# Performance work log

Hardware: AMD Instinct MI355X
Metric: run time of the kernel (lower is better)

Reference implementation:

```python
import jax, jax.numpy as jnp
import numpy as np

HIDDEN = 1024
NUM_EXPERTS = 8
TOP_K = 2
BATCH, SEQ = 4, 2048


def setup_inputs() -> dict:
    key = jax.random.key(0)
    ks = jax.random.split(key, 7)
    s = 0.02
    x = jax.random.normal(ks[0], (BATCH, SEQ, HIDDEN), dtype=jnp.float32)
    Wr = jax.random.normal(ks[1], (HIDDEN, NUM_EXPERTS), dtype=jnp.float32) * s
    br = jnp.zeros((NUM_EXPERTS,), dtype=jnp.float32)
    W1 = jax.random.normal(ks[2], (NUM_EXPERTS, HIDDEN, 2 * HIDDEN), dtype=jnp.float32) * s
    b1 = jnp.zeros((NUM_EXPERTS, 2 * HIDDEN), dtype=jnp.float32)
    W2 = jax.random.normal(ks[3], (NUM_EXPERTS, 2 * HIDDEN, HIDDEN), dtype=jnp.float32) * s
    b2 = jnp.zeros((NUM_EXPERTS, HIDDEN), dtype=jnp.float32)
    return {"x": x, "Wr": Wr, "br": br, "W1": W1, "b1": b1, "W2": W2, "b2": b2}


def reference(x, Wr, br, W1, b1, W2, b2):
    # Router: softmax over experts, take top-k, renormalize top-k weights.
    logits = jnp.einsum('bsh,he->bse', x, Wr) + br              # [B,S,E]
    routing = jax.nn.softmax(logits, axis=-1)
    topw, topi = jax.lax.top_k(routing, TOP_K)                   # [B,S,K]
    topw = jax.nn.softmax(topw, axis=-1)
    # Dense all-expert MLP (same math as masked gather/scatter combine).
    h = jnp.einsum('bsh,ehf->bsef', x, W1) + b1                  # [B,S,E,2H]
    h = jax.nn.gelu(h, approximate=False)                        # torch GELU = exact erf
    y = jnp.einsum('bsef,efh->bseh', h, W2) + b2                 # [B,S,E,H]
    # Per-token expert combine weights: sum_k onehot(topi_k)*topw_k -> [B,S,E]
    scale = jnp.sum(jax.nn.one_hot(topi, NUM_EXPERTS, dtype=x.dtype) * topw[..., None], axis=-2)
    return jnp.einsum('bse,bseh->bsh', scale, y)
```

## Files before the change

kernel.cpp:

```cpp
#include <hip/hip_runtime.h>
#include <math.h>

#define HID 1024
#define FF  2048
#define NE  8
#define NT  8192

typedef __attribute__((ext_vector_type(4))) float f32x4;
typedef __bf16 bf16x8 __attribute__((ext_vector_type(8)));

#define GLL(g, l) __builtin_amdgcn_global_load_lds( \
    (const __attribute__((address_space(1))) unsigned int*)(g), \
    (__attribute__((address_space(3))) unsigned int*)(l), 16, 0, 0)

static __device__ __forceinline__ ushort f2b(float f){
  union { float f; unsigned int u; } v; v.f = f;
  unsigned int r = (v.u + 0x7FFFu + ((v.u >> 16) & 1u)) >> 16;
  return (ushort)r;
}

__global__ __launch_bounds__(256) void k_cvt_x(const float* __restrict__ x,
                                               ushort* __restrict__ xb){
  size_t i8 = ((size_t)blockIdx.x * 256 + threadIdx.x) * 8;
  const float* s = x + i8;
  ushort o[8];
  #pragma unroll
  for (int j = 0; j < 8; ++j) o[j] = f2b(s[j]);
  *(uint4*)(xb + i8) = *(uint4*)o;
}

__global__ __launch_bounds__(256) void k_transpose(
    const float* __restrict__ src, ushort* __restrict__ dst, int K, int N){
  __shared__ __align__(16) ushort Tt[64][72];
  int e = blockIdx.z;
  int n0 = blockIdx.x * 64, k0 = blockIdx.y * 64;
  int t = threadIdx.x;
  int r = t >> 2, c = (t & 3) * 16;
  const float* s = src + (size_t)e*K*N + (size_t)(k0+r)*N + n0 + c;
  #pragma unroll
  for (int q = 0; q < 4; ++q){
    float4 v = *(const float4*)(s + q*4);
    Tt[r][c+q*4+0] = f2b(v.x); Tt[r][c+q*4+1] = f2b(v.y);
    Tt[r][c+q*4+2] = f2b(v.z); Tt[r][c+q*4+3] = f2b(v.w);
  }
  __syncthreads();
  ushort tmp[16];
  #pragma unroll
  for (int i = 0; i < 16; ++i) tmp[i] = Tt[c+i][r];
  ushort* d = dst + (size_t)e*N*K + (size_t)(n0+r)*K + k0 + c;
  *(uint4*)(d)     = *(uint4*)&tmp[0];
  *(uint4*)(d + 8) = *(uint4*)&tmp[8];
}

__global__ __launch_bounds__(256) void k_router(
    const float* __restrict__ x, const float* __restrict__ Wr,
    const float* __restrict__ br, int* __restrict__ topi,
    float* __restrict__ topw){
  __shared__ __align__(16) float sW[HID*NE];
  int tid = threadIdx.x;
  const uint4* srcW = (const uint4*)Wr;
  uint4* dstW = (uint4*)sW;
  #pragma unroll
  for (int i = 0; i < 8; ++i) dstW[tid*8+i] = srcW[tid*8+i];
  __syncthreads();
  int wave = tid >> 6, lane = tid & 63;
  int t = blockIdx.x * 4 + wave;
  const float* xrow = x + (size_t)t * HID;
  double acc[NE];
  #pragma unroll
  for (int e=0;e<NE;++e) acc[e]=0.0;
  for (int it = 0; it < HID/64; ++it){
    int h = it*64 + lane;
    double xv = (double)xrow[h];
    #pragma unroll
    for (int e=0;e<NE;++e) acc[e] += xv * (double)sW[h*NE+e];
  }
  #pragma unroll
  for (int off=32; off>0; off>>=1){
    #pragma unroll
    for (int e=0;e<NE;++e) acc[e] += __shfl_down(acc[e], off, 64);
  }
  if (lane == 0){
    double lg[NE], p[NE];
    double m = -1e300;
    #pragma unroll
    for (int e=0;e<NE;++e){ lg[e] = acc[e] + (double)br[e]; m = fmax(m, lg[e]); }
    double s = 0.0;
    #pragma unroll
    for (int e=0;e<NE;++e){ p[e] = exp(lg[e]-m); s += p[e]; }
    double inv = 1.0 / s;
    #pragma unroll
    for (int e=0;e<NE;++e) p[e] *= inv;
    int i0 = 0;
    #pragma unroll
    for (int e=1;e<NE;++e) if (p[e] > p[i0]) i0 = e;
    int i1 = -1;
    #pragma unroll
    for (int e=0;e<NE;++e){ if (e==i0) continue; if (i1 < 0 || p[e] > p[i1]) i1 = e; }
    double d = exp(p[i1] - p[i0]);
    topi[t*2+0] = i0; topi[t*2+1] = i1;
    topw[t*2+0] = (float)(1.0 / (1.0 + d));
    topw[t*2+1] = (float)(d / (1.0 + d));
  }
}

__global__ __launch_bounds__(256) void k_count(
    const int* __restrict__ topi, int* __restrict__ counts){
  __shared__ int lcnt[NE];
  int tid = threadIdx.x;
  if (tid < NE) lcnt[tid] = 0;
  __syncthreads();
  int t = blockIdx.x * 256 + tid;
  atomicAdd(&lcnt[topi[t*2+0]], 1);
  atomicAdd(&lcnt[topi[t*2+1]], 1);
  __syncthreads();
  if (tid < NE) atomicAdd(&counts[tid], lcnt[tid]);
}

__global__ void k_offsets(const int* __restrict__ counts, int* __restrict__ offsets,
                          int* __restrict__ cursor){
  if (threadIdx.x == 0 && blockIdx.x == 0){
    int run = 0;
    for (int e=0;e<NE;++e){ offsets[e] = run; cursor[e] = run; run += counts[e]; }
  }
}

__global__ __launch_bounds__(256) void k_fill(
    const int* __restrict__ topi, const float* __restrict__ topw, int* __restrict__ cursor,
    int* __restrict__ tok_of, float* __restrict__ w_of){
  __shared__ int lcnt[NE];
  __shared__ int lbase[NE];
  int tid = threadIdx.x;
  if (tid < NE) lcnt[tid] = 0;
  __syncthreads();
  int t = blockIdx.x * 256 + tid;
  int e0 = topi[t*2+0], e1 = topi[t*2+1];
  int p0 = atomicAdd(&lcnt[e0], 1);
  int p1 = atomicAdd(&lcnt[e1], 1);
  __syncthreads();
  if (tid < NE) lbase[tid] = atomicAdd(&cursor[tid], lcnt[tid]);
  __syncthreads();
  int pos0 = lbase[e0] + p0;
  tok_of[pos0] = t; w_of[pos0] = topw[t*2+0];
  int pos1 = lbase[e1] + p1;
  tok_of[pos1] = t; w_of[pos1] = topw[t*2+1];
}

__global__ __launch_bounds__(256) void k_gemm1(
    const ushort* __restrict__ x, const ushort* __restrict__ w1t, const float* __restrict__ b1,
    const int* __restrict__ tok_of, const int* __restrict__ offsets, const int* __restrict__ counts,
    ushort* __restrict__ hbuf){
  int e = blockIdx.z;
  int cnt = counts[e];
  int m0 = blockIdx.y * 128;
  if (m0 >= cnt) return;
  int n0 = blockIdx.x * 128;
  int base = offsets[e];
  __shared__ __align__(16) ushort As[128][32];
  __shared__ __align__(16) ushort Bs[128][32];
  int tid = threadIdx.x;
  int wave = tid >> 6, lane = tid & 63;
  int srow0 = wave*32 + (lane >> 2);
  int srow1 = srow0 + 16;
  int chunk = (lane & 3) * 8;
  int t0 = tok_of[base + min(m0 + srow0, cnt-1)];
  int t1 = tok_of[base + min(m0 + srow1, cnt-1)];
  const ushort* agp0 = x + (size_t)t0*HID + chunk;
  const ushort* agp1 = x + (size_t)t1*HID + chunk;
  const ushort* wb = w1t + (size_t)e*FF*HID;
  const ushort* bgp0 = wb + (size_t)(n0 + srow0)*HID + chunk;
  const ushort* bgp1 = wb + (size_t)(n0 + srow1)*HID + chunk;
  ushort* alds0 = &As[wave*32][0];
  ushort* alds1 = &As[wave*32+16][0];
  ushort* blds0 = &Bs[wave*32][0];
  ushort* blds1 = &Bs[wave*32+16][0];
  f32x4 acc[4][4];
  #pragma unroll
  for (int i=0;i<4;++i)
    #pragma unroll
    for (int j=0;j<4;++j){ acc[i][j][0]=0.f; acc[i][j][1]=0.f; acc[i][j][2]=0.f; acc[i][j][3]=0.f; }
  int wr = (wave >> 1) * 64, wc = (wave & 1) * 64;
  int lrow = lane & 15, quad = lane >> 4;
  for (int kk = 0; kk < HID; kk += 32){
    GLL(agp0 + kk, alds0);
    GLL(agp1 + kk, alds1);
    GLL(bgp0 + kk, blds0);
    GLL(bgp1 + kk, blds1);
    __syncthreads();
    bf16x8 af[4], bfr[4];
    #pragma unroll
    for (int i=0;i<4;++i) af[i]  = *(const bf16x8*)&As[wr + i*16 + lrow][quad*8];
    #pragma unroll
    for (int j=0;j<4;++j) bfr[j] = *(const bf16x8*)&Bs[wc + j*16 + lrow][quad*8];
    #pragma unroll
    for (int i=0;i<4;++i)
      #pragma unroll
      for (int j=0;j<4;++j)
        acc[i][j] = __builtin_amdgcn_mfma_f32_16x16x32_bf16(af[i], bfr[j], acc[i][j], 0, 0, 0);
    __syncthreads();
  }
  #pragma unroll
  for (int i=0;i<4;++i){
    #pragma unroll
    for (int rr=0; rr<4; ++rr){
      int mrel = wr + i*16 + quad*4 + rr;
      if (m0 + mrel < cnt){
        size_t grow = (size_t)(base + m0 + mrel) * FF;
        #pragma unroll
        for (int j=0;j<4;++j){
          int n = n0 + wc + j*16 + lrow;
          float v = acc[i][j][rr] + b1[e*FF + n];
          float g = 0.5f * v * (1.0f + erff(v * 0.70710678118654752f));
          hbuf[grow + n] = f2b(g);
        }
      }
    }
  }
}

__global__ __launch_bounds__(256) void k_gemm2(
    const ushort* __restrict__ hbuf, const ushort* __restrict__ w2t, const float* __restrict__ b2,
    const int* __restrict__ tok_of, const float* __restrict__ w_of,
    const int* __restrict__ offsets, const int* __restrict__ counts,
    float* __restrict__ outp){
  int e = blockIdx.z;
  int cnt = counts[e];
  int m0 = blockIdx.y * 128;
  if (m0 >= cnt) return;
  int n0 = blockIdx.x * 128;
  int base = offsets[e];
  __shared__ __align__(16) ushort As[128][32];
  __shared__ __align__(16) ushort Bs[128][32];
  int tid = threadIdx.x;
  int wave = tid >> 6, lane = tid & 63;
  int srow0 = wave*32 + (lane >> 2);
  int srow1 = srow0 + 16;
  int chunk = (lane & 3) * 8;
  int ar0 = base + min(m0 + srow0, cnt-1);
  int ar1 = base + min(m0 + srow1, cnt-1);
  const ushort* agp0 = hbuf + (size_t)ar0*FF + chunk;
  const ushort* agp1 = hbuf + (size_t)ar1*FF + chunk;
  const ushort* wb = w2t + (size_t)e*HID*FF;
  const ushort* bgp0 = wb + (size_t)(n0 + srow0)*FF + chunk;
  const ushort* bgp1 = wb + (size_t)(n0 + srow1)*FF + chunk;
  ushort* alds0 = &As[wave*32][0];
  ushort* alds1 = &As[wave*32+16][0];
  ushort* blds0 = &Bs[wave*32][0];
  ushort* blds1 = &Bs[wave*32+16][0];
  f32x4 acc[4][4];
  #pragma unroll
  for (int i=0;i<4;++i)
    #pragma unroll
    for (int j=0;j<4;++j){ acc[i][j][0]=0.f; acc[i][j][1]=0.f; acc[i][j][2]=0.f; acc[i][j][3]=0.f; }
  int wr = (wave >> 1) * 64, wc = (wave & 1) * 64;
  int lrow = lane & 15, quad = lane >> 4;
  for (int kk = 0; kk < FF; kk += 32){
    GLL(agp0 + kk, alds0);
    GLL(agp1 + kk, alds1);
    GLL(bgp0 + kk, blds0);
    GLL(bgp1 + kk, blds1);
    __syncthreads();
    bf16x8 af[4], bfr[4];
    #pragma unroll
    for (int i=0;i<4;++i) af[i]  = *(const bf16x8*)&As[wr + i*16 + lrow][quad*8];
    #pragma unroll
    for (int j=0;j<4;++j) bfr[j] = *(const bf16x8*)&Bs[wc + j*16 + lrow][quad*8];
    #pragma unroll
    for (int i=0;i<4;++i)
      #pragma unroll
      for (int j=0;j<4;++j)
        acc[i][j] = __builtin_amdgcn_mfma_f32_16x16x32_bf16(af[i], bfr[j], acc[i][j], 0, 0, 0);
    __syncthreads();
  }
  #pragma unroll
  for (int i=0;i<4;++i){
    #pragma unroll
    for (int rr=0; rr<4; ++rr){
      int mrel = wr + i*16 + quad*4 + rr;
      if (m0 + mrel < cnt){
        int pos = base + m0 + mrel;
        int tok = tok_of[pos];
        float wgt = w_of[pos];
        float* orow = outp + (size_t)tok * HID;
        #pragma unroll
        for (int j=0;j<4;++j){
          int n = n0 + wc + j*16 + lrow;
          float y = acc[i][j][rr] + b2[e*HID + n];
          atomicAdd(&orow[n], wgt * y);
        }
      }
    }
  }
}

extern "C" void kernel_launch(void* const* d_in, const int* in_sizes, int n_in,
                              void* d_out, int out_size, void* d_ws, size_t ws_size,
                              hipStream_t stream) {
  const float* x  = (const float*)d_in[0];
  const float* Wr = (const float*)d_in[1];
  const float* br = (const float*)d_in[2];
  const float* W1 = (const float*)d_in[3];
  const float* b1 = (const float*)d_in[4];
  const float* W2 = (const float*)d_in[5];
  const float* b2 = (const float*)d_in[6];
  float* out = (float*)d_out;

  char* w = (char*)d_ws;
  int*   counts  = (int*)(w + 0);
  int*   cursor  = (int*)(w + 64);
  int*   offsets = (int*)(w + 128);
  int*   topi    = (int*)(w + 131072);
  float* topw    = (float*)(w + 196608);
  int*   tok_of  = (int*)(w + 262144);
  float* w_of    = (float*)(w + 327680);
  const size_t XB_OFF  = 524288ull;
  const size_t W1T_OFF = XB_OFF  + 16ull*1024*1024;
  const size_t W2T_OFF = W1T_OFF + 32ull*1024*1024;
  const size_t HB_OFF  = W2T_OFF + 32ull*1024*1024;
  ushort* xb   = (ushort*)(w + XB_OFF);
  ushort* W1t  = (ushort*)(w + W1T_OFF);
  ushort* W2t  = (ushort*)(w + W2T_OFF);
  ushort* hbuf = (ushort*)(w + HB_OFF);

  hipMemsetAsync(w, 0, 256, stream);
  hipMemsetAsync(out, 0, (size_t)NT*HID*sizeof(float), stream);

  k_cvt_x<<<4096, 256, 0, stream>>>(x, xb);
  k_transpose<<<dim3(FF/64, HID/64, NE), 256, 0, stream>>>(W1, W1t, HID, FF);
  k_transpose<<<dim3(HID/64, FF/64, NE), 256, 0, stream>>>(W2, W2t, FF, HID);

  k_router<<<NT/4, 256, 0, stream>>>(x, Wr, br, topi, topw);
  k_count<<<NT/256, 256, 0, stream>>>(topi, counts);
  k_offsets<<<1, 64, 0, stream>>>(counts, offsets, cursor);
  k_fill<<<NT/256, 256, 0, stream>>>(topi, topw, cursor, tok_of, w_of);

  k_gemm1<<<dim3(FF/128, NT/128, NE), 256, 0, stream>>>(xb, W1t, b1, tok_of, offsets, counts, hbuf);
  k_gemm2<<<dim3(HID/128, NT/128, NE), 256, 0, stream>>>(hbuf, W2t, b2, tok_of, w_of, offsets, counts, out);
}
```

Before: 552.4 us.

## Compact expert tile scheduling and double-buffer LDS loads in MoE GEMMs

Builds a compact list of (expert, row-tile) pairs in the offsets kernel so both grouped GEMMs launch only about 136 live row tiles instead of a 64x8 grid where most blocks exit early. It also double-buffers the LDS tiles: the next K-slice is loaded asynchronously while the current one feeds MFMA, and one of the two barriers per iteration is removed. This is meant to cut launch and idle-block overhead and to hide global-load latency, at the cost of doubled LDS use per block. The single-barrier scheme relies on the barrier at the top of each iteration to order buffer reuse.

```diff
diff --git a/kernel.cpp b/kernel.cpp
--- a/kernel.cpp
+++ b/kernel.cpp
@@ -5,6 +5,7 @@
 #define FF  2048
 #define NE  8
 #define NT  8192
+#define MAXTILE 160
 
 typedef __attribute__((ext_vector_type(4))) float f32x4;
 typedef __bf16 bf16x8 __attribute__((ext_vector_type(8)));
@@ -118,10 +119,16 @@
 }
 
 __global__ void k_offsets(const int* __restrict__ counts, int* __restrict__ offsets,
-                          int* __restrict__ cursor){
+                          int* __restrict__ cursor, int* __restrict__ tile_e,
+                          int* __restrict__ tile_m, int* __restrict__ ntiles){
   if (threadIdx.x == 0 && blockIdx.x == 0){
-    int run = 0;
-    for (int e=0;e<NE;++e){ offsets[e] = run; cursor[e] = run; run += counts[e]; }
+    int run = 0, nt = 0;
+    for (int e=0;e<NE;++e){
+      offsets[e] = run; cursor[e] = run;
+      for (int m0 = 0; m0 < counts[e]; m0 += 128){ tile_e[nt] = e; tile_m[nt] = m0; ++nt; }
+      run += counts[e];
+    }
+    *ntiles = nt;
   }
 }
 
@@ -149,15 +156,17 @@
 __global__ __launch_bounds__(256) void k_gemm1(
     const ushort* __restrict__ x, const ushort* __restrict__ w1t, const float* __restrict__ b1,
     const int* __restrict__ tok_of, const int* __restrict__ offsets, const int* __restrict__ counts,
+    const int* __restrict__ tile_e, const int* __restrict__ tile_m, const int* __restrict__ ntiles,
     ushort* __restrict__ hbuf){
-  int e = blockIdx.z;
+  int ty = blockIdx.y;
+  if (ty >= *ntiles) return;
+  int e = tile_e[ty];
+  int m0 = tile_m[ty];
   int cnt = counts[e];
-  int m0 = blockIdx.y * 128;
-  if (m0 >= cnt) return;
+  int base = offsets[e];
   int n0 = blockIdx.x * 128;
-  int base = offsets[e];
-  __shared__ __align__(16) ushort As[128][32];
-  __shared__ __align__(16) ushort Bs[128][32];
+  __shared__ __align__(16) ushort As[2][128][32];
+  __shared__ __align__(16) ushort Bs[2][128][32];
   int tid = threadIdx.x;
   int wave = tid >> 6, lane = tid & 63;
   int srow0 = wave*32 + (lane >> 2);
@@ -170,10 +179,6 @@
   const ushort* wb = w1t + (size_t)e*FF*HID;
   const ushort* bgp0 = wb + (size_t)(n0 + srow0)*HID + chunk;
   const ushort* bgp1 = wb + (size_t)(n0 + srow1)*HID + chunk;
-  ushort* alds0 = &As[wave*32][0];
-  ushort* alds1 = &As[wave*32+16][0];
-  ushort* blds0 = &Bs[wave*32][0];
-  ushort* blds1 = &Bs[wave*32+16][0];
   f32x4 acc[4][4];
   #pragma unroll
   for (int i=0;i<4;++i)
@@ -181,23 +186,31 @@
     for (int j=0;j<4;++j){ acc[i][j][0]=0.f; acc[i][j][1]=0.f; acc[i][j][2]=0.f; acc[i][j][3]=0.f; }
   int wr = (wave >> 1) * 64, wc = (wave & 1) * 64;
   int lrow = lane & 15, quad = lane >> 4;
+  GLL(agp0, &As[0][wave*32][0]);
+  GLL(agp1, &As[0][wave*32+16][0]);
+  GLL(bgp0, &Bs[0][wave*32][0]);
+  GLL(bgp1, &Bs[0][wave*32+16][0]);
+  int cur = 0;
   for (int kk = 0; kk < HID; kk += 32){
-    GLL(agp0 + kk, alds0);
-    GLL(agp1 + kk, alds1);
-    GLL(bgp0 + kk, blds0);
-    GLL(bgp1 + kk, blds1);
     __syncthreads();
+    int nxt = cur ^ 1;
+    if (kk + 32 < HID){
+      GLL(agp0 + kk + 32, &As[nxt][wave*32][0]);
+      GLL(agp1 + kk + 32, &As[nxt][wave*32+16][0]);
+      GLL(bgp0 + kk + 32, &Bs[nxt][wave*32][0]);
+      GLL(bgp1 + kk + 32, &Bs[nxt][wave*32+16][0]);
+    }
     bf16x8 af[4], bfr[4];
     #pragma unroll
-    for (int i=0;i<4;++i) af[i]  = *(const bf16x8*)&As[wr + i*16 + lrow][quad*8];
-    #pragma unroll
-    for (int j=0;j<4;++j) bfr[j] = *(const bf16x8*)&Bs[wc + j*16 + lrow][quad*8];
+    for (int i=0;i<4;++i) af[i]  = *(const bf16x8*)&As[cur][wr + i*16 + lrow][quad*8];
+    #pragma unroll
+    for (int j=0;j<4;++j) bfr[j] = *(const bf16x8*)&Bs[cur][wc + j*16 + lrow][quad*8];
     #pragma unroll
     for (int i=0;i<4;++i)
       #pragma unroll
       for (int j=0;j<4;++j)
         acc[i][j] = __builtin_amdgcn_mfma_f32_16x16x32_bf16(af[i], bfr[j], acc[i][j], 0, 0, 0);
-    __syncthreads();
+    cur = nxt;
   }
   #pragma unroll
   for (int i=0;i<4;++i){
@@ -222,15 +235,17 @@
     const ushort* __restrict__ hbuf, const ushort* __restrict__ w2t, const float* __restrict__ b2,
     const int* __restrict__ tok_of, const float* __restrict__ w_of,
     const int* __restrict__ offsets, const int* __restrict__ counts,
+    const int* __restrict__ tile_e, const int* __restrict__ tile_m, const int* __restrict__ ntiles,
     float* __restrict__ outp){
-  int e = blockIdx.z;
+  int ty = blockIdx.y;
+  if (ty >= *ntiles) return;
+  int e = tile_e[ty];
+  int m0 = tile_m[ty];
   int cnt = counts[e];
-  int m0 = blockIdx.y * 128;
-  if (m0 >= cnt) return;
+  int base = offsets[e];
   int n0 = blockIdx.x * 128;
-  int base = offsets[e];
-  __shared__ __align__(16) ushort As[128][32];
-  __shared__ __align__(16) ushort Bs[128][32];
+  __shared__ __align__(16) ushort As[2][128][32];
+  __shared__ __align__(16) ushort Bs[2][128][32];
   int tid = threadIdx.x;
   int wave = tid >> 6, lane = tid & 63;
   int srow0 = wave*32 + (lane >> 2);
@@ -243,10 +258,6 @@
   const ushort* wb = w2t + (size_t)e*HID*FF;
   const ushort* bgp0 = wb + (size_t)(n0 + srow0)*FF + chunk;
   const ushort* bgp1 = wb + (size_t)(n0 + srow1)*FF + chunk;
-  ushort* alds0 = &As[wave*32][0];
-  ushort* alds1 = &As[wave*32+16][0];
-  ushort* blds0 = &Bs[wave*32][0];
-  ushort* blds1 = &Bs[wave*32+16][0];
   f32x4 acc[4][4];
   #pragma unroll
   for (int i=0;i<4;++i)
@@ -254,23 +265,31 @@
     for (int j=0;j<4;++j){ acc[i][j][0]=0.f; acc[i][j][1]=0.f; acc[i][j][2]=0.f; acc[i][j][3]=0.f; }
   int wr = (wave >> 1) * 64, wc = (wave & 1) * 64;
   int lrow = lane & 15, quad = lane >> 4;
+  GLL(agp0, &As[0][wave*32][0]);
+  GLL(agp1, &As[0][wave*32+16][0]);
+  GLL(bgp0, &Bs[0][wave*32][0]);
+  GLL(bgp1, &Bs[0][wave*32+16][0]);
+  int cur = 0;
   for (int kk = 0; kk < FF; kk += 32){
-    GLL(agp0 + kk, alds0);
-    GLL(agp1 + kk, alds1);
-    GLL(bgp0 + kk, blds0);
-    GLL(bgp1 + kk, blds1);
     __syncthreads();
+    int nxt = cur ^ 1;
+    if (kk + 32 < FF){
+      GLL(agp0 + kk + 32, &As[nxt][wave*32][0]);
+      GLL(agp1 + kk + 32, &As[nxt][wave*32+16][0]);
+      GLL(bgp0 + kk + 32, &Bs[nxt][wave*32][0]);
+      GLL(bgp1 + kk + 32, &Bs[nxt][wave*32+16][0]);
+    }
     bf16x8 af[4], bfr[4];
     #pragma unroll
-    for (int i=0;i<4;++i) af[i]  = *(const bf16x8*)&As[wr + i*16 + lrow][quad*8];
-    #pragma unroll
-    for (int j=0;j<4;++j) bfr[j] = *(const bf16x8*)&Bs[wc + j*16 + lrow][quad*8];
+    for (int i=0;i<4;++i) af[i]  = *(const bf16x8*)&As[cur][wr + i*16 + lrow][quad*8];
+    #pragma unroll
+    for (int j=0;j<4;++j) bfr[j] = *(const bf16x8*)&Bs[cur][wc + j*16 + lrow][quad*8];
     #pragma unroll
     for (int i=0;i<4;++i)
       #pragma unroll
       for (int j=0;j<4;++j)
         acc[i][j] = __builtin_amdgcn_mfma_f32_16x16x32_bf16(af[i], bfr[j], acc[i][j], 0, 0, 0);
-    __syncthreads();
+    cur = nxt;
   }
   #pragma unroll
   for (int i=0;i<4;++i){
@@ -309,6 +328,9 @@
   int*   counts  = (int*)(w + 0);
   int*   cursor  = (int*)(w + 64);
   int*   offsets = (int*)(w + 128);
+  int*   ntiles  = (int*)(w + 192);
+  int*   tile_e  = (int*)(w + 1024);
+  int*   tile_m  = (int*)(w + 1024 + MAXTILE*4);
   int*   topi    = (int*)(w + 131072);
   float* topw    = (float*)(w + 196608);
   int*   tok_of  = (int*)(w + 262144);
@@ -331,9 +353,11 @@
 
   k_router<<<NT/4, 256, 0, stream>>>(x, Wr, br, topi, topw);
   k_count<<<NT/256, 256, 0, stream>>>(topi, counts);
-  k_offsets<<<1, 64, 0, stream>>>(counts, offsets, cursor);
+  k_offsets<<<1, 64, 0, stream>>>(counts, offsets, cursor, tile_e, tile_m, ntiles);
   k_fill<<<NT/256, 256, 0, stream>>>(topi, topw, cursor, tok_of, w_of);
 
-  k_gemm1<<<dim3(FF/128, NT/128, NE), 256, 0, stream>>>(xb, W1t, b1, tok_of, offsets, counts, hbuf);
-  k_gemm2<<<dim3(HID/128, NT/128, NE), 256, 0, stream>>>(hbuf, W2t, b2, tok_of, w_of, offsets, counts, out);
-}
+  k_gemm1<<<dim3(FF/128, MAXTILE), 256, 0, stream>>>(xb, W1t, b1, tok_of, offsets, counts,
+                                                     tile_e, tile_m, ntiles, hbuf);
+  k_gemm2<<<dim3(HID/128, MAXTILE), 256, 0, stream>>>(hbuf, W2t, b2, tok_of, w_of, offsets, counts,
+                                                      tile_e, tile_m, ntiles, out);
+}
```

Measured after the change: 568.0 us. 2.8% more time.
